# Optimization experiments

Measured on AMD Instinct MI355X. Metric: run time of the kernel, lower is better.

## Reference

```python
import jax, jax.numpy as jnp
import numpy as np

EPS_OT = 0.1        # args.model.ot_reg
N_ITERS = 5         # args.model.ot_transport
COS_EPS = 1e-8      # torch F.cosine_similarity eps
L2_EPS = 1e-12      # torch F.normalize eps
LN_EPS = 1e-5       # nn.LayerNorm default eps
IN_DIM, HID = 768, 256


def setup_inputs() -> dict:
    key = jax.random.key(0)
    ks = jax.random.split(key, 8)
    Ba, Bb, Sa, Sb = 48, 48, 96, 96
    s_in = 1.0 / np.sqrt(IN_DIM)
    return {
        "batch_a": jax.random.normal(ks[0], (Ba, Sa, IN_DIM), jnp.float32),
        "batch_b": jax.random.normal(ks[1], (Bb, Sb, IN_DIM), jnp.float32),
        "Wq": jax.random.normal(ks[2], (IN_DIM, HID), jnp.float32) * s_in,
        "bq": jnp.zeros((HID,), jnp.float32),
        "Wk": jax.random.normal(ks[3], (IN_DIM, HID), jnp.float32) * s_in,
        "bk": jnp.zeros((HID,), jnp.float32),
        "Wv": jax.random.normal(ks[4], (IN_DIM, HID), jnp.float32) * s_in,
        "bv": jnp.zeros((HID,), jnp.float32),
        "ln_g": jnp.ones((HID,), jnp.float32),
        "ln_b": jnp.zeros((HID,), jnp.float32),
    }


def _layernorm(x, g, b):
    mu = jnp.mean(x, axis=-1, keepdims=True)
    var = jnp.var(x, axis=-1, keepdims=True)
    return (x - mu) * jax.lax.rsqrt(var + LN_EPS) * g + b


def _sinkhorn(C):
    # multiplicative Sinkhorn on kernel exp(C/eps); row/col renormalization
    T = jnp.exp(C / EPS_OT)  # [Ba,Bb,Sa,Sb]
    def body(_, T):
        T = T / jnp.sum(T, axis=-1, keepdims=True)
        T = T / jnp.sum(T, axis=-2, keepdims=True)
        return T
    return jax.lax.fori_loop(0, N_ITERS, body, T)


def reference(batch_a, batch_b, Wq, bq, Wk, bk, Wv, bv, ln_g, ln_b):
    q = batch_a @ Wq + bq          # [Ba,Sa,H]
    k = batch_b @ Wk + bk          # [Bb,Sb,H]
    v = batch_b @ Wv + bv          # [Bb,Sb,H]

    # cosine similarity across batches: [Ba,Bb,Sa,Sb]
    qn = q / jnp.maximum(jnp.linalg.norm(q, axis=-1, keepdims=True), COS_EPS)
    kn = k / jnp.maximum(jnp.linalg.norm(k, axis=-1, keepdims=True), COS_EPS)
    C = jnp.einsum('aid,bjd->abij', qn, kn)

    T = jax.lax.stop_gradient(_sinkhorn(C))  # C.detach() in source
    # F.normalize(dim=-1): L2 over last dim
    T = T / jnp.maximum(jnp.linalg.norm(T, axis=-1, keepdims=True), L2_EPS)
    # dropout p=0.0 -> identity (eval)

    attended = jnp.einsum('abij,bjd->abid', T, v) + q[:, None]  # [Ba,Bb,Sa,H]
    return _layernorm(attended, ln_g, ln_b)
```

## Files before the change

### kernel.cpp

```cpp
#include <hip/hip_runtime.h>
#include <hip/hip_bf16.h>

typedef __attribute__((ext_vector_type(4))) float f32x4;
typedef __attribute__((ext_vector_type(2))) float f32x2;
typedef __attribute__((ext_vector_type(8))) short bf16x8;
typedef __attribute__((ext_vector_type(4))) short s16x4;

#define BA 48
#define BB 48
#define SS 96
#define DIN 768
#define HH 256

static __device__ __forceinline__ short f2bf(float f) {
    __hip_bfloat16 h = __float2bfloat16(f);
    return *reinterpret_cast<short*>(&h);
}

static __device__ __forceinline__ f32x4 mfma16(bf16x8 a, bf16x8 b, f32x4 c) {
    return __builtin_amdgcn_mfma_f32_16x16x32_bf16(a, b, c, 0, 0, 0);
}

__global__ __launch_bounds__(256) void wt_kernel(
    const float* __restrict__ Wq, const float* __restrict__ Wk,
    const float* __restrict__ Wv, short* __restrict__ wt) {
    __shared__ float tile[64][65];
    int k0 = blockIdx.x * 64, n0 = blockIdx.y * 64, mat = blockIdx.z;
    const float* W = (mat == 0) ? Wq : (mat == 1) ? Wk : Wv;
    int t = threadIdx.x;
#pragma unroll
    for (int j = 0; j < 16; ++j) {
        int kk = j * 4 + (t >> 6);
        int nn = t & 63;
        tile[kk][nn] = W[(size_t)(k0 + kk) * HH + n0 + nn];
    }
    __syncthreads();
#pragma unroll
    for (int j = 0; j < 4; ++j) {
        int nn = j * 16 + (t >> 4);
        int kk = (t & 15) * 4;
        s16x4 pk;
#pragma unroll
        for (int i = 0; i < 4; ++i) pk[i] = f2bf(tile[kk + i][nn]);
        *reinterpret_cast<s16x4*>(&wt[(size_t)(mat * HH + n0 + nn) * DIN + k0 + kk]) = pk;
    }
}

__global__ __launch_bounds__(256) void xbf_kernel(
    const float* __restrict__ Xa, const float* __restrict__ Xb,
    short* __restrict__ xa, short* __restrict__ xb) {
    size_t i = (size_t)blockIdx.x * 256 + threadIdx.x;
    const float* src;
    short* dst;
    size_t off;
    if (i < 442368) { src = Xa; dst = xa; off = i * 8; }
    else            { src = Xb; dst = xb; off = (i - 442368) * 8; }
    f32x4 a = *reinterpret_cast<const f32x4*>(src + off);
    f32x4 b = *reinterpret_cast<const f32x4*>(src + off + 4);
    bf16x8 o;
    o[0] = f2bf(a[0]); o[1] = f2bf(a[1]); o[2] = f2bf(a[2]); o[3] = f2bf(a[3]);
    o[4] = f2bf(b[0]); o[5] = f2bf(b[1]); o[6] = f2bf(b[2]); o[7] = f2bf(b[3]);
    *reinterpret_cast<bf16x8*>(dst + off) = o;
}

__global__ __launch_bounds__(384) void qkv_kernel(
    const short* __restrict__ xa, const short* __restrict__ xb,
    const float* __restrict__ bq, const float* __restrict__ bk, const float* __restrict__ bv,
    const short* __restrict__ wt,
    float* __restrict__ q_ws, float* __restrict__ k_ws, short* __restrict__ vt_ws) {
    __shared__ short vtile[32][104];

    int bb = blockIdx.x;
    int mat = blockIdx.y;
    int c0 = blockIdx.z * 32;
    int tid = threadIdx.x;
    int wave = tid >> 6, lane = tid & 63;
    int c = lane & 15, g = lane >> 4;

    const short* X = ((mat == 0) ? xa : xb) + (size_t)bb * SS * DIN;
    const short* Wt = wt + (size_t)mat * HH * DIN;
    const float* bias = (mat == 0) ? bq : (mat == 1) ? bk : bv;

    const f32x4 z4 = {0.f, 0.f, 0.f, 0.f};
    f32x4 acc[2];
    acc[0] = z4; acc[1] = z4;

    const short* ap = X + (16 * wave + c) * DIN + g * 8;
    const short* bp = Wt + (c0 + c) * DIN + g * 8;
    for (int kk = 0; kk < DIN; kk += 32) {
        bf16x8 af = *reinterpret_cast<const bf16x8*>(ap + kk);
#pragma unroll
        for (int n = 0; n < 2; ++n) {
            bf16x8 bf = *reinterpret_cast<const bf16x8*>(bp + n * 16 * DIN + kk);
            acc[n] = mfma16(af, bf, acc[n]);
        }
    }
#pragma unroll
    for (int n = 0; n < 2; ++n) {
        float bv_ = bias[c0 + n * 16 + c];
#pragma unroll
        for (int r = 0; r < 4; ++r) acc[n][r] += bv_;
    }

    if (mat < 2) {
        float* dst = (mat == 0) ? q_ws : k_ws;
#pragma unroll
        for (int n = 0; n < 2; ++n)
#pragma unroll
            for (int r = 0; r < 4; ++r)
                dst[(bb * SS + 16 * wave + 4 * g + r) * HH + c0 + n * 16 + c] = acc[n][r];
    } else {
#pragma unroll
        for (int n = 0; n < 2; ++n)
#pragma unroll
            for (int r = 0; r < 4; ++r)
                vtile[n * 16 + c][16 * wave + 4 * g + r] = f2bf(acc[n][r]);
        __syncthreads();
        {
            int t = tid;
            int d = t / 12, ch = t % 12;
            bf16x8 pk = *reinterpret_cast<const bf16x8*>(&vtile[d][ch * 8]);
            *reinterpret_cast<bf16x8*>(vt_ws + ((size_t)(bb * HH) + c0 + d) * SS + ch * 8) = pk;
        }
    }
}

__global__ __launch_bounds__(256) void norm_kernel(
    const float* __restrict__ q_ws, const float* __restrict__ k_ws,
    short* __restrict__ qn_ws, short* __restrict__ kn_ws) {
    int row = blockIdx.x * 4 + (threadIdx.x >> 6);
    int lane = threadIdx.x & 63;
    int isq = (row < 4608);
    const float* src = isq ? q_ws : k_ws;
    short* dst = isq ? qn_ws : kn_ws;
    int r = isq ? row : row - 4608;

    f32x4 v = *reinterpret_cast<const f32x4*>(src + (size_t)r * HH + lane * 4);
    float s = v[0] * v[0] + v[1] * v[1] + v[2] * v[2] + v[3] * v[3];
#pragma unroll
    for (int m = 1; m < 64; m <<= 1) s += __shfl_xor(s, m);
    float inv = 1.0f / fmaxf(sqrtf(s), 1e-8f);
    s16x4 o;
#pragma unroll
    for (int j = 0; j < 4; ++j) o[j] = f2bf(v[j] * inv);
    *reinterpret_cast<s16x4*>(dst + (size_t)r * HH + lane * 4) = o;
}

__global__ __launch_bounds__(256, 2) void sink_kernel(
    const short* __restrict__ qn_ws, const short* __restrict__ kn_ws,
    short* __restrict__ t_ws, int a_off) {
    int wave = threadIdx.x >> 6, lane = threadIdx.x & 63;
    int c = lane & 15, g = lane >> 4;
    int b = blockIdx.x * 4 + wave;
    int al = blockIdx.y;
    int a = al + a_off;

    const short* qbase = qn_ws + (size_t)(a * SS) * HH + c * HH + g * 8;
    const short* kbase = kn_ws + (size_t)(b * SS) * HH + c * HH + g * 8;

    const f32x4 z4 = {0.f, 0.f, 0.f, 0.f};
    f32x4 K[6][6];
#pragma unroll
    for (int ti = 0; ti < 6; ++ti)
#pragma unroll
        for (int tj = 0; tj < 6; ++tj) K[ti][tj] = z4;

#pragma unroll
    for (int kk = 0; kk < 8; ++kk) {
        bf16x8 qf[6];
#pragma unroll
        for (int ti = 0; ti < 6; ++ti)
            qf[ti] = *reinterpret_cast<const bf16x8*>(qbase + ti * 16 * HH + kk * 32);
#pragma unroll
        for (int tj = 0; tj < 6; ++tj) {
            bf16x8 kf = *reinterpret_cast<const bf16x8*>(kbase + tj * 16 * HH + kk * 32);
#pragma unroll
            for (int ti = 0; ti < 6; ++ti)
                K[ti][tj] = mfma16(kf, qf[ti], K[ti][tj]);
        }
    }

#pragma unroll
    for (int ti = 0; ti < 6; ++ti)
#pragma unroll
        for (int tj = 0; tj < 6; ++tj)
#pragma unroll
            for (int r = 0; r < 4; ++r)
                K[ti][tj][r] = exp2f(K[ti][tj][r] * 14.4269504088896341f);

    f32x4 v[6];
#pragma unroll
    for (int tj = 0; tj < 6; ++tj) v[tj] = (f32x4){1.f, 1.f, 1.f, 1.f};
    float u[6];

#pragma unroll 1
    for (int it = 0; it < 5; ++it) {
#pragma unroll
        for (int ti = 0; ti < 6; ++ti) {
            f32x4 p0 = K[ti][0] * v[0] + K[ti][1] * v[1];
            f32x4 p1 = K[ti][2] * v[2] + K[ti][3] * v[3];
            f32x4 p2 = K[ti][4] * v[4] + K[ti][5] * v[5];
            f32x4 p = (p0 + p1) + p2;
            float rs = (p[0] + p[1]) + (p[2] + p[3]);
            rs += __shfl_xor(rs, 16);
            rs += __shfl_xor(rs, 32);
            u[ti] = 1.0f / rs;
        }
#pragma unroll
        for (int tj = 0; tj < 6; ++tj) {
            f32x4 c0 = K[0][tj] * u[0] + K[1][tj] * u[1];
            f32x4 c1 = K[2][tj] * u[2] + K[3][tj] * u[3];
            f32x4 c2 = K[4][tj] * u[4] + K[5][tj] * u[5];
            f32x4 cs = (c0 + c1) + c2;
#pragma unroll
            for (int m = 1; m < 16; m <<= 1)
#pragma unroll
                for (int r = 0; r < 4; ++r) cs[r] += __shfl_xor(cs[r], m);
#pragma unroll
            for (int r = 0; r < 4; ++r) v[tj][r] = 1.0f / cs[r];
        }
    }

    short* tp = t_ws + (size_t)(al * BB + b) * SS * SS;
#pragma unroll
    for (int ti = 0; ti < 6; ++ti) {
        f32x4 w[6];
#pragma unroll
        for (int tj = 0; tj < 6; ++tj) w[tj] = K[ti][tj] * v[tj];
        f32x4 q0 = w[0] * w[0] + w[1] * w[1];
        f32x4 q1 = w[2] * w[2] + w[3] * w[3];
        f32x4 q2 = w[4] * w[4] + w[5] * w[5];
        f32x4 qq = (q0 + q1) + q2;
        float ss = (qq[0] + qq[1]) + (qq[2] + qq[3]);
        ss += __shfl_xor(ss, 16);
        ss += __shfl_xor(ss, 32);
        float linv = 1.0f / fmaxf(sqrtf(ss), 1e-12f);
#pragma unroll
        for (int tj = 0; tj < 6; ++tj) {
            s16x4 pk;
#pragma unroll
            for (int r = 0; r < 4; ++r) pk[r] = f2bf(w[tj][r] * linv);
            *reinterpret_cast<s16x4*>(tp + (16 * ti + c) * SS + 16 * tj + 4 * g) = pk;
        }
    }
}

__global__ __launch_bounds__(512) void pv_kernel(
    const short* __restrict__ t_ws, const short* __restrict__ vt_ws,
    const float* __restrict__ q_ws,
    const float* __restrict__ ln_g, const float* __restrict__ ln_b,
    float* __restrict__ out, int a_off) {
    __shared__ float wstats[8][2][SS];

    int b = blockIdx.x, al = blockIdx.y;
    int a = al + a_off;
    int tid = threadIdx.x;
    int w = tid >> 6, lane = tid & 63;
    int c = lane & 15, g = lane >> 4;
    int d0 = w * 32;

    const f32x4 z4 = {0.f, 0.f, 0.f, 0.f};
    f32x4 acc[2][6];
#pragma unroll
    for (int dt = 0; dt < 2; ++dt)
#pragma unroll
        for (int ti = 0; ti < 6; ++ti) acc[dt][ti] = z4;

    const short* vp = vt_ws + ((size_t)(b * HH) + d0 + c) * SS + g * 8;
    const short* tp = t_ws + ((size_t)(al * BB + b)) * SS * SS + c * SS + g * 8;
#pragma unroll
    for (int ks = 0; ks < 3; ++ks) {
        bf16x8 af0 = *reinterpret_cast<const bf16x8*>(vp + ks * 32);
        bf16x8 af1 = *reinterpret_cast<const bf16x8*>(vp + 16 * SS + ks * 32);
#pragma unroll
        for (int ti = 0; ti < 6; ++ti) {
            bf16x8 bf = *reinterpret_cast<const bf16x8*>(tp + ti * 16 * SS + ks * 32);
            acc[0][ti] = mfma16(af0, bf, acc[0][ti]);
            acc[1][ti] = mfma16(af1, bf, acc[1][ti]);
        }
    }

    const float* qa = q_ws + (size_t)a * SS * HH;
#pragma unroll
    for (int ti = 0; ti < 6; ++ti) {
        int i = 16 * ti + c;
        f32x4 q0 = *reinterpret_cast<const f32x4*>(qa + (size_t)i * HH + d0 + 4 * g);
        f32x4 q1 = *reinterpret_cast<const f32x4*>(qa + (size_t)i * HH + d0 + 16 + 4 * g);
        f32x4 x0 = acc[0][ti] + q0;
        f32x4 x1 = acc[1][ti] + q1;
        acc[0][ti] = x0;
        acc[1][ti] = x1;
        f32x4 sv = x0 + x1;
        f32x4 qv = x0 * x0 + x1 * x1;
        float l1 = (sv[0] + sv[1]) + (sv[2] + sv[3]);
        float l2 = (qv[0] + qv[1]) + (qv[2] + qv[3]);
        l1 += __shfl_xor(l1, 16);
        l1 += __shfl_xor(l1, 32);
        l2 += __shfl_xor(l2, 16);
        l2 += __shfl_xor(l2, 32);
        if (g == 0) {
            wstats[w][0][i] = l1;
            wstats[w][1][i] = l2;
        }
    }
    __syncthreads();

    f32x4 g4[2], b4[2];
#pragma unroll
    for (int dt = 0; dt < 2; ++dt) {
        g4[dt] = *reinterpret_cast<const f32x4*>(ln_g + d0 + dt * 16 + 4 * g);
        b4[dt] = *reinterpret_cast<const f32x4*>(ln_b + d0 + dt * 16 + 4 * g);
    }

    float* ob = out + ((size_t)(a * BB + b)) * SS * HH;
#pragma unroll
    for (int ti = 0; ti < 6; ++ti) {
        int i = 16 * ti + c;
        float t1 = ((wstats[0][0][i] + wstats[1][0][i]) + (wstats[2][0][i] + wstats[3][0][i])) +
                   ((wstats[4][0][i] + wstats[5][0][i]) + (wstats[6][0][i] + wstats[7][0][i]));
        float t2 = ((wstats[0][1][i] + wstats[1][1][i]) + (wstats[2][1][i] + wstats[3][1][i])) +
                   ((wstats[4][1][i] + wstats[5][1][i]) + (wstats[6][1][i] + wstats[7][1][i]));
        float mean = t1 * (1.0f / 256.0f);
        float var = t2 * (1.0f / 256.0f) - mean * mean;
        float inv = rsqrtf(var + 1e-5f);
#pragma unroll
        for (int dt = 0; dt < 2; ++dt) {
            f32x4 x = acc[dt][ti];
            f32x4 o;
#pragma unroll
            for (int r = 0; r < 4; ++r)
                o[r] = (x[r] - mean) * inv * g4[dt][r] + b4[dt][r];
            *reinterpret_cast<f32x4*>(ob + (size_t)i * HH + d0 + dt * 16 + 4 * g) = o;
        }
    }
}

extern "C" void kernel_launch(void* const* d_in, const int* in_sizes, int n_in,
                              void* d_out, int out_size, void* d_ws, size_t ws_size,
                              hipStream_t stream) {
    const float* Xa = (const float*)d_in[0];
    const float* Xb = (const float*)d_in[1];
    const float* Wq = (const float*)d_in[2];
    const float* bq = (const float*)d_in[3];
    const float* Wk = (const float*)d_in[4];
    const float* bk = (const float*)d_in[5];
    const float* Wv = (const float*)d_in[6];
    const float* bv = (const float*)d_in[7];
    const float* ln_g = (const float*)d_in[8];
    const float* ln_b = (const float*)d_in[9];
    float* out = (float*)d_out;

    char* ws = (char*)d_ws;
    short* wt    = (short*)(ws);
    short* xa_bf = (short*)(ws + 1179648);
    short* xb_bf = (short*)(ws + 8257536);
    float* q_ws  = (float*)(ws + 15335424);
    float* k_ws  = (float*)(ws + 20054016);
    short* qn_ws = (short*)(ws + 24772608);
    short* kn_ws = (short*)(ws + 27131904);
    short* vt_ws = (short*)(ws + 29491200);

    const size_t t_full = (size_t)BA * BB * SS * SS * 2;
    size_t t_off = 31850496;
    size_t avail = (ws_size > t_off) ? ws_size - t_off : 0;
    int nch;
    if (avail >= t_full) nch = 1;
    else if (avail >= t_full / 2) nch = 2;
    else if (avail >= t_full / 4) nch = 4;
    else { nch = 4; t_off = 0; }
    short* t_ws = (short*)(ws + t_off);
    int apc = BA / nch;

    wt_kernel<<<dim3(12, 4, 3), dim3(256), 0, stream>>>(Wq, Wk, Wv, wt);
    xbf_kernel<<<dim3(3456), dim3(256), 0, stream>>>(Xa, Xb, xa_bf, xb_bf);
    qkv_kernel<<<dim3(BA, 3, 8), dim3(384), 0, stream>>>(xa_bf, xb_bf, bq, bk, bv, wt,
                                                         q_ws, k_ws, vt_ws);
    norm_kernel<<<dim3(2304), dim3(256), 0, stream>>>(q_ws, k_ws, qn_ws, kn_ws);
    for (int ch = 0; ch < nch; ++ch) {
        sink_kernel<<<dim3(12, apc), dim3(256), 0, stream>>>(qn_ws, kn_ws, t_ws, ch * apc);
        pv_kernel<<<dim3(BB, apc), dim3(512), 0, stream>>>(t_ws, vt_ws, q_ws,
                                                           ln_g, ln_b, out, ch * apc);
    }
}
```

Measured before the change: 241.1 us.

## Fuse Sinkhorn and PV+LayerNorm into one kernel keeping T in LDS

Merges the Sinkhorn kernel and the PV/LayerNorm kernel into one kernel. Each wave computes a full (a,b) transport plan, writes it as bf16 to shared memory, then loops over all 256 hidden dims in 32-wide chunks for PV and LayerNorm. This removes the global round-trip of the large T tensor and the chunked launches. The PV MFMAs run twice, once for the statistics and once for the output, so fewer threads do more serial work. The weight-transpose and input-cast kernels are also merged into one launch.

```diff
diff --git a/kernel.cpp b/kernel.cpp
--- a/kernel.cpp
+++ b/kernel.cpp
@@ -2,7 +2,6 @@
 #include <hip/hip_bf16.h>
 
 typedef __attribute__((ext_vector_type(4))) float f32x4;
-typedef __attribute__((ext_vector_type(2))) float f32x2;
 typedef __attribute__((ext_vector_type(8))) short bf16x8;
 typedef __attribute__((ext_vector_type(4))) short s16x4;
 
@@ -21,46 +20,50 @@
     return __builtin_amdgcn_mfma_f32_16x16x32_bf16(a, b, c, 0, 0, 0);
 }
 
-__global__ __launch_bounds__(256) void wt_kernel(
+__global__ __launch_bounds__(256) void prep_kernel(
+    const float* __restrict__ Xa, const float* __restrict__ Xb,
     const float* __restrict__ Wq, const float* __restrict__ Wk,
-    const float* __restrict__ Wv, short* __restrict__ wt) {
+    const float* __restrict__ Wv,
+    short* __restrict__ xa, short* __restrict__ xb, short* __restrict__ wt) {
     __shared__ float tile[64][65];
-    int k0 = blockIdx.x * 64, n0 = blockIdx.y * 64, mat = blockIdx.z;
-    const float* W = (mat == 0) ? Wq : (mat == 1) ? Wk : Wv;
-    int t = threadIdx.x;
-#pragma unroll
-    for (int j = 0; j < 16; ++j) {
-        int kk = j * 4 + (t >> 6);
-        int nn = t & 63;
-        tile[kk][nn] = W[(size_t)(k0 + kk) * HH + n0 + nn];
-    }
-    __syncthreads();
-#pragma unroll
-    for (int j = 0; j < 4; ++j) {
-        int nn = j * 16 + (t >> 4);
-        int kk = (t & 15) * 4;
-        s16x4 pk;
-#pragma unroll
-        for (int i = 0; i < 4; ++i) pk[i] = f2bf(tile[kk + i][nn]);
-        *reinterpret_cast<s16x4*>(&wt[(size_t)(mat * HH + n0 + nn) * DIN + k0 + kk]) = pk;
-    }
-}
-
-__global__ __launch_bounds__(256) void xbf_kernel(
-    const float* __restrict__ Xa, const float* __restrict__ Xb,
-    short* __restrict__ xa, short* __restrict__ xb) {
-    size_t i = (size_t)blockIdx.x * 256 + threadIdx.x;
-    const float* src;
-    short* dst;
-    size_t off;
-    if (i < 442368) { src = Xa; dst = xa; off = i * 8; }
-    else            { src = Xb; dst = xb; off = (i - 442368) * 8; }
-    f32x4 a = *reinterpret_cast<const f32x4*>(src + off);
-    f32x4 b = *reinterpret_cast<const f32x4*>(src + off + 4);
-    bf16x8 o;
-    o[0] = f2bf(a[0]); o[1] = f2bf(a[1]); o[2] = f2bf(a[2]); o[3] = f2bf(a[3]);
-    o[4] = f2bf(b[0]); o[5] = f2bf(b[1]); o[6] = f2bf(b[2]); o[7] = f2bf(b[3]);
-    *reinterpret_cast<bf16x8*>(dst + off) = o;
+    int bx = blockIdx.x;
+    if (bx < 3456) {
+        size_t i = (size_t)bx * 256 + threadIdx.x;
+        const float* src;
+        short* dst;
+        size_t off;
+        if (i < 442368) { src = Xa; dst = xa; off = i * 8; }
+        else            { src = Xb; dst = xb; off = (i - 442368) * 8; }
+        f32x4 a = *reinterpret_cast<const f32x4*>(src + off);
+        f32x4 b = *reinterpret_cast<const f32x4*>(src + off + 4);
+        bf16x8 o;
+        o[0] = f2bf(a[0]); o[1] = f2bf(a[1]); o[2] = f2bf(a[2]); o[3] = f2bf(a[3]);
+        o[4] = f2bf(b[0]); o[5] = f2bf(b[1]); o[6] = f2bf(b[2]); o[7] = f2bf(b[3]);
+        *reinterpret_cast<bf16x8*>(dst + off) = o;
+    } else {
+        int tt = bx - 3456;
+        int k0 = (tt % 12) * 64;
+        int n0 = ((tt / 12) % 4) * 64;
+        int mat = tt / 48;
+        const float* W = (mat == 0) ? Wq : (mat == 1) ? Wk : Wv;
+        int t = threadIdx.x;
+#pragma unroll
+        for (int j = 0; j < 16; ++j) {
+            int kk = j * 4 + (t >> 6);
+            int nn = t & 63;
+            tile[kk][nn] = W[(size_t)(k0 + kk) * HH + n0 + nn];
+        }
+        __syncthreads();
+#pragma unroll
+        for (int j = 0; j < 4; ++j) {
+            int nn = j * 16 + (t >> 4);
+            int kk = (t & 15) * 4;
+            s16x4 pk;
+#pragma unroll
+            for (int i = 0; i < 4; ++i) pk[i] = f2bf(tile[kk + i][nn]);
+            *reinterpret_cast<s16x4*>(&wt[(size_t)(mat * HH + n0 + nn) * DIN + k0 + kk]) = pk;
+        }
+    }
 }
 
 __global__ __launch_bounds__(384) void qkv_kernel(
@@ -146,19 +149,23 @@
     *reinterpret_cast<s16x4*>(dst + (size_t)r * HH + lane * 4) = o;
 }
 
-__global__ __launch_bounds__(256, 2) void sink_kernel(
+__global__ __launch_bounds__(128, 2) void fused_kernel(
     const short* __restrict__ qn_ws, const short* __restrict__ kn_ws,
-    short* __restrict__ t_ws, int a_off) {
+    const float* __restrict__ q_ws, const short* __restrict__ vt_ws,
+    const float* __restrict__ ln_g, const float* __restrict__ ln_b,
+    float* __restrict__ out) {
+    __shared__ short Tl[2][SS][104];
+
     int wave = threadIdx.x >> 6, lane = threadIdx.x & 63;
     int c = lane & 15, g = lane >> 4;
-    int b = blockIdx.x * 4 + wave;
-    int al = blockIdx.y;
-    int a = al + a_off;
+    int b = blockIdx.x;
+    int a = blockIdx.y * 2 + wave;
 
     const short* qbase = qn_ws + (size_t)(a * SS) * HH + c * HH + g * 8;
     const short* kbase = kn_ws + (size_t)(b * SS) * HH + c * HH + g * 8;
 
     const f32x4 z4 = {0.f, 0.f, 0.f, 0.f};
+
     f32x4 K[6][6];
 #pragma unroll
     for (int ti = 0; ti < 6; ++ti)
@@ -221,7 +228,7 @@
         }
     }
 
-    short* tp = t_ws + (size_t)(al * BB + b) * SS * SS;
+    short* tp = &Tl[wave][0][0];
 #pragma unroll
     for (int ti = 0; ti < 6; ++ti) {
         f32x4 w[6];
@@ -240,97 +247,105 @@
             s16x4 pk;
 #pragma unroll
             for (int r = 0; r < 4; ++r) pk[r] = f2bf(w[tj][r] * linv);
-            *reinterpret_cast<s16x4*>(tp + (16 * ti + c) * SS + 16 * tj + 4 * g) = pk;
-        }
-    }
-}
-
-__global__ __launch_bounds__(512) void pv_kernel(
-    const short* __restrict__ t_ws, const short* __restrict__ vt_ws,
-    const float* __restrict__ q_ws,
-    const float* __restrict__ ln_g, const float* __restrict__ ln_b,
-    float* __restrict__ out, int a_off) {
-    __shared__ float wstats[8][2][SS];
-
-    int b = blockIdx.x, al = blockIdx.y;
-    int a = al + a_off;
-    int tid = threadIdx.x;
-    int w = tid >> 6, lane = tid & 63;
-    int c = lane & 15, g = lane >> 4;
-    int d0 = w * 32;
-
-    const f32x4 z4 = {0.f, 0.f, 0.f, 0.f};
-    f32x4 acc[2][6];
-#pragma unroll
-    for (int dt = 0; dt < 2; ++dt)
-#pragma unroll
-        for (int ti = 0; ti < 6; ++ti) acc[dt][ti] = z4;
-
-    const short* vp = vt_ws + ((size_t)(b * HH) + d0 + c) * SS + g * 8;
-    const short* tp = t_ws + ((size_t)(al * BB + b)) * SS * SS + c * SS + g * 8;
-#pragma unroll
-    for (int ks = 0; ks < 3; ++ks) {
-        bf16x8 af0 = *reinterpret_cast<const bf16x8*>(vp + ks * 32);
-        bf16x8 af1 = *reinterpret_cast<const bf16x8*>(vp + 16 * SS + ks * 32);
+            *reinterpret_cast<s16x4*>(tp + (16 * ti + c) * 104 + 16 * tj + 4 * g) = pk;
+        }
+    }
+
+    bf16x8 tf[6][3];
+#pragma unroll
+    for (int ti = 0; ti < 6; ++ti)
+#pragma unroll
+        for (int ks = 0; ks < 3; ++ks)
+            tf[ti][ks] = *reinterpret_cast<const bf16x8*>(
+                tp + (16 * ti + c) * 104 + 32 * ks + 8 * g);
+
+    const short* vp = vt_ws + ((size_t)(b * HH) + c) * SS + 8 * g;
+    const float* qa = q_ws + (size_t)a * SS * HH;
+
+    float s1[6], s2[6];
+#pragma unroll
+    for (int ti = 0; ti < 6; ++ti) { s1[ti] = 0.f; s2[ti] = 0.f; }
+
+#pragma unroll 1
+    for (int ch = 0; ch < 8; ++ch) {
+        int d0 = ch * 32;
+        f32x4 acc[2][6];
+#pragma unroll
+        for (int dt = 0; dt < 2; ++dt)
+#pragma unroll
+            for (int ti = 0; ti < 6; ++ti) acc[dt][ti] = z4;
+#pragma unroll
+        for (int ks = 0; ks < 3; ++ks) {
+            bf16x8 af0 = *reinterpret_cast<const bf16x8*>(vp + (size_t)d0 * SS + ks * 32);
+            bf16x8 af1 = *reinterpret_cast<const bf16x8*>(vp + (size_t)(d0 + 16) * SS + ks * 32);
+#pragma unroll
+            for (int ti = 0; ti < 6; ++ti) {
+                acc[0][ti] = mfma16(af0, tf[ti][ks], acc[0][ti]);
+                acc[1][ti] = mfma16(af1, tf[ti][ks], acc[1][ti]);
+            }
+        }
 #pragma unroll
         for (int ti = 0; ti < 6; ++ti) {
-            bf16x8 bf = *reinterpret_cast<const bf16x8*>(tp + ti * 16 * SS + ks * 32);
-            acc[0][ti] = mfma16(af0, bf, acc[0][ti]);
-            acc[1][ti] = mfma16(af1, bf, acc[1][ti]);
-        }
-    }
-
-    const float* qa = q_ws + (size_t)a * SS * HH;
+            int i = 16 * ti + c;
+#pragma unroll
+            for (int dt = 0; dt < 2; ++dt) {
+                f32x4 q4 = *reinterpret_cast<const f32x4*>(
+                    qa + (size_t)i * HH + d0 + 16 * dt + 4 * g);
+                f32x4 x = acc[dt][ti] + q4;
+                s1[ti] += (x[0] + x[1]) + (x[2] + x[3]);
+                f32x4 xx = x * x;
+                s2[ti] += (xx[0] + xx[1]) + (xx[2] + xx[3]);
+            }
+        }
+    }
+    float mean[6], inv[6];
 #pragma unroll
     for (int ti = 0; ti < 6; ++ti) {
-        int i = 16 * ti + c;
-        f32x4 q0 = *reinterpret_cast<const f32x4*>(qa + (size_t)i * HH + d0 + 4 * g);
-        f32x4 q1 = *reinterpret_cast<const f32x4*>(qa + (size_t)i * HH + d0 + 16 + 4 * g);
-        f32x4 x0 = acc[0][ti] + q0;
-        f32x4 x1 = acc[1][ti] + q1;
-        acc[0][ti] = x0;
-        acc[1][ti] = x1;
-        f32x4 sv = x0 + x1;
-        f32x4 qv = x0 * x0 + x1 * x1;
-        float l1 = (sv[0] + sv[1]) + (sv[2] + sv[3]);
-        float l2 = (qv[0] + qv[1]) + (qv[2] + qv[3]);
-        l1 += __shfl_xor(l1, 16);
-        l1 += __shfl_xor(l1, 32);
-        l2 += __shfl_xor(l2, 16);
-        l2 += __shfl_xor(l2, 32);
-        if (g == 0) {
-            wstats[w][0][i] = l1;
-            wstats[w][1][i] = l2;
-        }
-    }
-    __syncthreads();
-
-    f32x4 g4[2], b4[2];
-#pragma unroll
-    for (int dt = 0; dt < 2; ++dt) {
-        g4[dt] = *reinterpret_cast<const f32x4*>(ln_g + d0 + dt * 16 + 4 * g);
-        b4[dt] = *reinterpret_cast<const f32x4*>(ln_b + d0 + dt * 16 + 4 * g);
+        float t1 = s1[ti], t2 = s2[ti];
+        t1 += __shfl_xor(t1, 16);
+        t1 += __shfl_xor(t1, 32);
+        t2 += __shfl_xor(t2, 16);
+        t2 += __shfl_xor(t2, 32);
+        mean[ti] = t1 * (1.0f / 256.0f);
+        float var = t2 * (1.0f / 256.0f) - mean[ti] * mean[ti];
+        inv[ti] = rsqrtf(var + 1e-5f);
     }
 
     float* ob = out + ((size_t)(a * BB + b)) * SS * HH;
-#pragma unroll
-    for (int ti = 0; ti < 6; ++ti) {
-        int i = 16 * ti + c;
-        float t1 = ((wstats[0][0][i] + wstats[1][0][i]) + (wstats[2][0][i] + wstats[3][0][i])) +
-                   ((wstats[4][0][i] + wstats[5][0][i]) + (wstats[6][0][i] + wstats[7][0][i]));
-        float t2 = ((wstats[0][1][i] + wstats[1][1][i]) + (wstats[2][1][i] + wstats[3][1][i])) +
-                   ((wstats[4][1][i] + wstats[5][1][i]) + (wstats[6][1][i] + wstats[7][1][i]));
-        float mean = t1 * (1.0f / 256.0f);
-        float var = t2 * (1.0f / 256.0f) - mean * mean;
-        float inv = rsqrtf(var + 1e-5f);
+#pragma unroll 1
+    for (int ch = 0; ch < 8; ++ch) {
+        int d0 = ch * 32;
+        f32x4 acc[2][6];
+#pragma unroll
+        for (int dt = 0; dt < 2; ++dt)
+#pragma unroll
+            for (int ti = 0; ti < 6; ++ti) acc[dt][ti] = z4;
+#pragma unroll
+        for (int ks = 0; ks < 3; ++ks) {
+            bf16x8 af0 = *reinterpret_cast<const bf16x8*>(vp + (size_t)d0 * SS + ks * 32);
+            bf16x8 af1 = *reinterpret_cast<const bf16x8*>(vp + (size_t)(d0 + 16) * SS + ks * 32);
+#pragma unroll
+            for (int ti = 0; ti < 6; ++ti) {
+                acc[0][ti] = mfma16(af0, tf[ti][ks], acc[0][ti]);
+                acc[1][ti] = mfma16(af1, tf[ti][ks], acc[1][ti]);
+            }
+        }
 #pragma unroll
         for (int dt = 0; dt < 2; ++dt) {
-            f32x4 x = acc[dt][ti];
-            f32x4 o;
-#pragma unroll
-            for (int r = 0; r < 4; ++r)
-                o[r] = (x[r] - mean) * inv * g4[dt][r] + b4[dt][r];
-            *reinterpret_cast<f32x4*>(ob + (size_t)i * HH + d0 + dt * 16 + 4 * g) = o;
+            f32x4 g4 = *reinterpret_cast<const f32x4*>(ln_g + d0 + 16 * dt + 4 * g);
+            f32x4 b4 = *reinterpret_cast<const f32x4*>(ln_b + d0 + 16 * dt + 4 * g);
+#pragma unroll
+            for (int ti = 0; ti < 6; ++ti) {
+                int i = 16 * ti + c;
+                f32x4 q4 = *reinterpret_cast<const f32x4*>(
+                    qa + (size_t)i * HH + d0 + 16 * dt + 4 * g);
+                f32x4 x = acc[dt][ti] + q4;
+                f32x4 o;
+#pragma unroll
+                for (int r = 0; r < 4; ++r)
+                    o[r] = (x[r] - mean[ti]) * inv[ti] * g4[r] + b4[r];
+                *reinterpret_cast<f32x4*>(ob + (size_t)i * HH + d0 + 16 * dt + 4 * g) = o;
+            }
         }
     }
 }
@@ -360,25 +375,11 @@
     short* kn_ws = (short*)(ws + 27131904);
     short* vt_ws = (short*)(ws + 29491200);
 
-    const size_t t_full = (size_t)BA * BB * SS * SS * 2;
-    size_t t_off = 31850496;
-    size_t avail = (ws_size > t_off) ? ws_size - t_off : 0;
-    int nch;
-    if (avail >= t_full) nch = 1;
-    else if (avail >= t_full / 2) nch = 2;
-    else if (avail >= t_full / 4) nch = 4;
-    else { nch = 4; t_off = 0; }
-    short* t_ws = (short*)(ws + t_off);
-    int apc = BA / nch;
-
-    wt_kernel<<<dim3(12, 4, 3), dim3(256), 0, stream>>>(Wq, Wk, Wv, wt);
-    xbf_kernel<<<dim3(3456), dim3(256), 0, stream>>>(Xa, Xb, xa_bf, xb_bf);
+    prep_kernel<<<dim3(3600), dim3(256), 0, stream>>>(Xa, Xb, Wq, Wk, Wv,
+                                                      xa_bf, xb_bf, wt);
     qkv_kernel<<<dim3(BA, 3, 8), dim3(384), 0, stream>>>(xa_bf, xb_bf, bq, bk, bv, wt,
                                                          q_ws, k_ws, vt_ws);
     norm_kernel<<<dim3(2304), dim3(256), 0, stream>>>(q_ws, k_ws, qn_ws, kn_ws);
-    for (int ch = 0; ch < nch; ++ch) {
-        sink_kernel<<<dim3(12, apc), dim3(256), 0, stream>>>(qn_ws, kn_ws, t_ws, ch * apc);
-        pv_kernel<<<dim3(BB, apc), dim3(512), 0, stream>>>(t_ws, vt_ws, q_ws,
-                                                           ln_g, ln_b, out, ch * apc);
-    }
-}
+    fused_kernel<<<dim3(BB, BA / 2), dim3(128), 0, stream>>>(qn_ws, kn_ws, q_ws, vt_ws,
+                                                             ln_g, ln_b, out);
+}
```

After: 255.5 us. 1.06x slower.

## Pack Sinkhorn kernel tiles as bf16 pairs and process two query batches per wave

Applied to the files above, without the earlier changes.

A new sinkhorn kernel stores exp(C/eps) in registers as packed bf16 pairs, halving register footprint, so each wave can handle two query batches (a and a+24) against the same key block. This reuses the key fragments and halves the grid in y. The weight-transpose and input-conversion kernels are also merged into one launch to cut launch overhead. Storing the kernel matrix in bf16 loses precision in the Sinkhorn iterations, and the new path only runs when the full T workspace fits (nch==1).

```diff
diff --git a/kernel.cpp b/kernel.cpp
--- a/kernel.cpp
+++ b/kernel.cpp
@@ -2,7 +2,6 @@
 #include <hip/hip_bf16.h>
 
 typedef __attribute__((ext_vector_type(4))) float f32x4;
-typedef __attribute__((ext_vector_type(2))) float f32x2;
 typedef __attribute__((ext_vector_type(8))) short bf16x8;
 typedef __attribute__((ext_vector_type(4))) short s16x4;
 
@@ -17,50 +16,60 @@
     return *reinterpret_cast<short*>(&h);
 }
 
+static __device__ __forceinline__ unsigned pk2bf(float lo, float hi) {
+    return ((unsigned)(unsigned short)f2bf(hi) << 16) | (unsigned)(unsigned short)f2bf(lo);
+}
+static __device__ __forceinline__ float ubflo(unsigned p) { return __uint_as_float(p << 16); }
+static __device__ __forceinline__ float ubfhi(unsigned p) { return __uint_as_float(p & 0xffff0000u); }
+
 static __device__ __forceinline__ f32x4 mfma16(bf16x8 a, bf16x8 b, f32x4 c) {
     return __builtin_amdgcn_mfma_f32_16x16x32_bf16(a, b, c, 0, 0, 0);
 }
 
-__global__ __launch_bounds__(256) void wt_kernel(
+__global__ __launch_bounds__(256) void prep_kernel(
+    const float* __restrict__ Xa, const float* __restrict__ Xb,
     const float* __restrict__ Wq, const float* __restrict__ Wk,
-    const float* __restrict__ Wv, short* __restrict__ wt) {
+    const float* __restrict__ Wv,
+    short* __restrict__ xa, short* __restrict__ xb, short* __restrict__ wt) {
     __shared__ float tile[64][65];
-    int k0 = blockIdx.x * 64, n0 = blockIdx.y * 64, mat = blockIdx.z;
-    const float* W = (mat == 0) ? Wq : (mat == 1) ? Wk : Wv;
-    int t = threadIdx.x;
-#pragma unroll
-    for (int j = 0; j < 16; ++j) {
-        int kk = j * 4 + (t >> 6);
-        int nn = t & 63;
-        tile[kk][nn] = W[(size_t)(k0 + kk) * HH + n0 + nn];
-    }
-    __syncthreads();
-#pragma unroll
-    for (int j = 0; j < 4; ++j) {
-        int nn = j * 16 + (t >> 4);
-        int kk = (t & 15) * 4;
-        s16x4 pk;
-#pragma unroll
-        for (int i = 0; i < 4; ++i) pk[i] = f2bf(tile[kk + i][nn]);
-        *reinterpret_cast<s16x4*>(&wt[(size_t)(mat * HH + n0 + nn) * DIN + k0 + kk]) = pk;
-    }
-}
-
-__global__ __launch_bounds__(256) void xbf_kernel(
-    const float* __restrict__ Xa, const float* __restrict__ Xb,
-    short* __restrict__ xa, short* __restrict__ xb) {
-    size_t i = (size_t)blockIdx.x * 256 + threadIdx.x;
-    const float* src;
-    short* dst;
-    size_t off;
-    if (i < 442368) { src = Xa; dst = xa; off = i * 8; }
-    else            { src = Xb; dst = xb; off = (i - 442368) * 8; }
-    f32x4 a = *reinterpret_cast<const f32x4*>(src + off);
-    f32x4 b = *reinterpret_cast<const f32x4*>(src + off + 4);
-    bf16x8 o;
-    o[0] = f2bf(a[0]); o[1] = f2bf(a[1]); o[2] = f2bf(a[2]); o[3] = f2bf(a[3]);
-    o[4] = f2bf(b[0]); o[5] = f2bf(b[1]); o[6] = f2bf(b[2]); o[7] = f2bf(b[3]);
-    *reinterpret_cast<bf16x8*>(dst + off) = o;
+    int bx = blockIdx.x;
+    if (bx < 3456) {
+        size_t i = (size_t)bx * 256 + threadIdx.x;
+        const float* src;
+        short* dst;
+        size_t off;
+        if (i < 442368) { src = Xa; dst = xa; off = i * 8; }
+        else            { src = Xb; dst = xb; off = (i - 442368) * 8; }
+        f32x4 a = *reinterpret_cast<const f32x4*>(src + off);
+        f32x4 b = *reinterpret_cast<const f32x4*>(src + off + 4);
+        bf16x8 o;
+        o[0] = f2bf(a[0]); o[1] = f2bf(a[1]); o[2] = f2bf(a[2]); o[3] = f2bf(a[3]);
+        o[4] = f2bf(b[0]); o[5] = f2bf(b[1]); o[6] = f2bf(b[2]); o[7] = f2bf(b[3]);
+        *reinterpret_cast<bf16x8*>(dst + off) = o;
+    } else {
+        int tt = bx - 3456;
+        int k0 = (tt % 12) * 64;
+        int n0 = ((tt / 12) % 4) * 64;
+        int mat = tt / 48;
+        const float* W = (mat == 0) ? Wq : (mat == 1) ? Wk : Wv;
+        int t = threadIdx.x;
+#pragma unroll
+        for (int j = 0; j < 16; ++j) {
+            int kk = j * 4 + (t >> 6);
+            int nn = t & 63;
+            tile[kk][nn] = W[(size_t)(k0 + kk) * HH + n0 + nn];
+        }
+        __syncthreads();
+#pragma unroll
+        for (int j = 0; j < 4; ++j) {
+            int nn = j * 16 + (t >> 4);
+            int kk = (t & 15) * 4;
+            s16x4 pk;
+#pragma unroll
+            for (int i = 0; i < 4; ++i) pk[i] = f2bf(tile[kk + i][nn]);
+            *reinterpret_cast<s16x4*>(&wt[(size_t)(mat * HH + n0 + nn) * DIN + k0 + kk]) = pk;
+        }
+    }
 }
 
 __global__ __launch_bounds__(384) void qkv_kernel(
@@ -144,6 +153,128 @@
 #pragma unroll
     for (int j = 0; j < 4; ++j) o[j] = f2bf(v[j] * inv);
     *reinterpret_cast<s16x4*>(dst + (size_t)r * HH + lane * 4) = o;
+}
+
+__global__ __launch_bounds__(256, 2) void sink2_kernel(
+    const short* __restrict__ qn_ws, const short* __restrict__ kn_ws,
+    short* __restrict__ t_ws) {
+    int wave = threadIdx.x >> 6, lane = threadIdx.x & 63;
+    int c = lane & 15, g = lane >> 4;
+    int b = blockIdx.x * 4 + wave;
+    int al = blockIdx.y;
+
+    const short* kbase = kn_ws + (size_t)(b * SS) * HH + c * HH + g * 8;
+    const f32x4 z4 = {0.f, 0.f, 0.f, 0.f};
+    const float L2E10 = 14.4269504088896341f;
+
+    unsigned Kp[2][6][6][2];
+
+#pragma unroll
+    for (int p = 0; p < 2; ++p) {
+        const short* qbase = qn_ws + (size_t)((al + 24 * p) * SS) * HH + c * HH + g * 8;
+#pragma unroll
+        for (int ti = 0; ti < 6; ++ti) {
+            f32x4 acc[6];
+#pragma unroll
+            for (int tj = 0; tj < 6; ++tj) acc[tj] = z4;
+#pragma unroll
+            for (int kk = 0; kk < 8; ++kk) {
+                bf16x8 qf = *reinterpret_cast<const bf16x8*>(qbase + ti * 16 * HH + kk * 32);
+#pragma unroll
+                for (int tj = 0; tj < 6; ++tj) {
+                    bf16x8 kf = *reinterpret_cast<const bf16x8*>(kbase + tj * 16 * HH + kk * 32);
+                    acc[tj] = mfma16(kf, qf, acc[tj]);
+                }
+            }
+#pragma unroll
+            for (int tj = 0; tj < 6; ++tj) {
+                float e0 = exp2f(acc[tj][0] * L2E10);
+                float e1 = exp2f(acc[tj][1] * L2E10);
+                float e2 = exp2f(acc[tj][2] * L2E10);
+                float e3 = exp2f(acc[tj][3] * L2E10);
+                Kp[p][ti][tj][0] = pk2bf(e0, e1);
+                Kp[p][ti][tj][1] = pk2bf(e2, e3);
+            }
+        }
+    }
+
+    f32x4 v[2][6];
+#pragma unroll
+    for (int p = 0; p < 2; ++p)
+#pragma unroll
+        for (int tj = 0; tj < 6; ++tj) v[p][tj] = (f32x4){1.f, 1.f, 1.f, 1.f};
+    float u[2][6];
+
+#pragma unroll 1
+    for (int it = 0; it < 5; ++it) {
+#pragma unroll
+        for (int p = 0; p < 2; ++p)
+#pragma unroll
+            for (int ti = 0; ti < 6; ++ti) {
+                float rs0 = 0.f, rs1 = 0.f;
+#pragma unroll
+                for (int tj = 0; tj < 6; ++tj) {
+                    rs0 += ubflo(Kp[p][ti][tj][0]) * v[p][tj][0] +
+                           ubflo(Kp[p][ti][tj][1]) * v[p][tj][2];
+                    rs1 += ubfhi(Kp[p][ti][tj][0]) * v[p][tj][1] +
+                           ubfhi(Kp[p][ti][tj][1]) * v[p][tj][3];
+                }
+                float rs = rs0 + rs1;
+                rs += __shfl_xor(rs, 16);
+                rs += __shfl_xor(rs, 32);
+                u[p][ti] = 1.0f / rs;
+            }
+#pragma unroll
+        for (int p = 0; p < 2; ++p)
+#pragma unroll
+            for (int tj = 0; tj < 6; ++tj) {
+                f32x4 cs = z4;
+#pragma unroll
+                for (int ti = 0; ti < 6; ++ti) {
+                    cs[0] += ubflo(Kp[p][ti][tj][0]) * u[p][ti];
+                    cs[1] += ubfhi(Kp[p][ti][tj][0]) * u[p][ti];
+                    cs[2] += ubflo(Kp[p][ti][tj][1]) * u[p][ti];
+                    cs[3] += ubfhi(Kp[p][ti][tj][1]) * u[p][ti];
+                }
+#pragma unroll
+                for (int m = 1; m < 16; m <<= 1)
+#pragma unroll
+                    for (int r = 0; r < 4; ++r) cs[r] += __shfl_xor(cs[r], m);
+#pragma unroll
+                for (int r = 0; r < 4; ++r) v[p][tj][r] = 1.0f / cs[r];
+            }
+    }
+
+#pragma unroll
+    for (int p = 0; p < 2; ++p) {
+        short* tp = t_ws + (size_t)((al + 24 * p) * BB + b) * SS * SS;
+#pragma unroll
+        for (int ti = 0; ti < 6; ++ti) {
+            float ss0 = 0.f, ss1 = 0.f;
+#pragma unroll
+            for (int tj = 0; tj < 6; ++tj) {
+                float t0 = ubflo(Kp[p][ti][tj][0]) * v[p][tj][0];
+                float t1 = ubfhi(Kp[p][ti][tj][0]) * v[p][tj][1];
+                float t2 = ubflo(Kp[p][ti][tj][1]) * v[p][tj][2];
+                float t3 = ubfhi(Kp[p][ti][tj][1]) * v[p][tj][3];
+                ss0 += t0 * t0 + t2 * t2;
+                ss1 += t1 * t1 + t3 * t3;
+            }
+            float ss = ss0 + ss1;
+            ss += __shfl_xor(ss, 16);
+            ss += __shfl_xor(ss, 32);
+            float linv = 1.0f / fmaxf(sqrtf(ss), 1e-12f);
+#pragma unroll
+            for (int tj = 0; tj < 6; ++tj) {
+                s16x4 pk;
+                pk[0] = f2bf(ubflo(Kp[p][ti][tj][0]) * v[p][tj][0] * linv);
+                pk[1] = f2bf(ubfhi(Kp[p][ti][tj][0]) * v[p][tj][1] * linv);
+                pk[2] = f2bf(ubflo(Kp[p][ti][tj][1]) * v[p][tj][2] * linv);
+                pk[3] = f2bf(ubfhi(Kp[p][ti][tj][1]) * v[p][tj][3] * linv);
+                *reinterpret_cast<s16x4*>(tp + (16 * ti + c) * SS + 16 * tj + 4 * g) = pk;
+            }
+        }
+    }
 }
 
 __global__ __launch_bounds__(256, 2) void sink_kernel(
@@ -371,14 +502,20 @@
     short* t_ws = (short*)(ws + t_off);
     int apc = BA / nch;
 
-    wt_kernel<<<dim3(12, 4, 3), dim3(256), 0, stream>>>(Wq, Wk, Wv, wt);
-    xbf_kernel<<<dim3(3456), dim3(256), 0, stream>>>(Xa, Xb, xa_bf, xb_bf);
+    prep_kernel<<<dim3(3600), dim3(256), 0, stream>>>(Xa, Xb, Wq, Wk, Wv,
+                                                      xa_bf, xb_bf, wt);
     qkv_kernel<<<dim3(BA, 3, 8), dim3(384), 0, stream>>>(xa_bf, xb_bf, bq, bk, bv, wt,
                                                          q_ws, k_ws, vt_ws);
     norm_kernel<<<dim3(2304), dim3(256), 0, stream>>>(q_ws, k_ws, qn_ws, kn_ws);
-    for (int ch = 0; ch < nch; ++ch) {
-        sink_kernel<<<dim3(12, apc), dim3(256), 0, stream>>>(qn_ws, kn_ws, t_ws, ch * apc);
-        pv_kernel<<<dim3(BB, apc), dim3(512), 0, stream>>>(t_ws, vt_ws, q_ws,
-                                                           ln_g, ln_b, out, ch * apc);
-    }
-}
+    if (nch == 1) {
+        sink2_kernel<<<dim3(12, 24), dim3(256), 0, stream>>>(qn_ws, kn_ws, t_ws);
+        pv_kernel<<<dim3(BB, BA), dim3(512), 0, stream>>>(t_ws, vt_ws, q_ws,
+                                                          ln_g, ln_b, out, 0);
+    } else {
+        for (int ch = 0; ch < nch; ++ch) {
+            sink_kernel<<<dim3(12, apc), dim3(256), 0, stream>>>(qn_ws, kn_ws, t_ws, ch * apc);
+            pv_kernel<<<dim3(BB, apc), dim3(512), 0, stream>>>(t_ws, vt_ws, q_ws,
+                                                               ln_g, ln_b, out, ch * apc);
+        }
+    }
+}
```

Measured after the change: 426.9 us. +77.1%, slower.
